# Kernel tuning notes

Measured on AMD Instinct MI355X. Metric: run time of the kernel, lower is better.

## Reference

```python
import jax, jax.numpy as jnp
import numpy as np

NK, NV, DK, DV = 16, 32, 128, 128
R = NV // NK
KCONV, CHUNK = 4, 64
KEY_DIM, VALUE_DIM = NK * DK, NV * DV
CONV_DIM = 2 * KEY_DIM + VALUE_DIM
HIDDEN = 2048
B, S = 1, 4096


def _l2norm(x, eps=1e-6):
    return x * jax.lax.rsqrt(jnp.sum(x * x, -1, keepdims=True) + eps)


def _causal_dwconv(x, w):
    # x: [B, C, S], w: [C, K]; depthwise causal conv (pad K-1 on left),
    # equivalent to torch F.conv1d(groups=C, padding=K-1)[..., :S]
    K = w.shape[-1]
    T = x.shape[-1]
    xp = jnp.pad(x, ((0, 0), (0, 0), (K - 1, 0)))
    out = jnp.zeros_like(x)
    for j in range(K):  # fixed tiny kernel taps
        out = out + w[None, :, j, None] * xp[:, :, j:j + T]
    return out


def _chunk_gated_delta_rule(q, k, v, g, beta):
    # q,k: [B,S,H,DK], v: [B,S,H,DV], g,beta: [B,S,H]; S % CHUNK == 0
    dtype0 = q.dtype
    q = _l2norm(q)
    k = _l2norm(k)
    tr = lambda x: jnp.swapaxes(x, 1, 2).astype(jnp.float32)
    q, k, v = tr(q), tr(k), tr(v)
    g = jnp.swapaxes(g, 1, 2).astype(jnp.float32)
    beta = jnp.swapaxes(beta, 1, 2).astype(jnp.float32)
    Bb, H, T, dk = k.shape
    dv = v.shape[-1]
    N = T // CHUNK
    q = q * dk ** -0.5
    v_beta = v * beta[..., None]
    k_beta = k * beta[..., None]
    resh = lambda x: x.reshape(Bb, H, N, CHUNK, x.shape[-1])
    q, k, v, k_beta, v_beta = map(resh, (q, k, v, k_beta, v_beta))
    g = jnp.cumsum(g.reshape(Bb, H, N, CHUNK), axis=-1)
    lo = jnp.tril(jnp.ones((CHUNK, CHUNK), bool))
    lo_strict = jnp.tril(jnp.ones((CHUNK, CHUNK), bool), -1)
    gdiff = g[..., :, None] - g[..., None, :]
    decay = jnp.where(lo, jnp.exp(jnp.where(lo, gdiff, 0.0)), 0.0)  # [B,H,N,C,C]
    # strictly-lower M = tril_{-1}(k_beta @ k^T * decay); the original in-chunk
    # forward-substitution loop computes exactly (I + M)^{-1}
    M = jnp.where(lo_strict, jnp.einsum('bhnik,bhnjk->bhnij', k_beta, k) * decay, 0.0)
    eye = jnp.eye(CHUNK, dtype=jnp.float32)
    T_inv = jax.scipy.linalg.solve_triangular(
        eye + M, jnp.broadcast_to(eye, M.shape), lower=True, unit_diagonal=True)
    v_c = jnp.einsum('bhnij,bhnjv->bhniv', T_inv, v_beta)
    k_cumdecay = jnp.einsum('bhnij,bhnjk->bhnik', T_inv, k_beta * jnp.exp(g)[..., None])
    attn_local = jnp.where(lo, jnp.einsum('bhnik,bhnjk->bhnij', q, k) * decay, 0.0)
    mv = lambda x: jnp.moveaxis(x, 2, 0)  # chunk axis to front for scan
    xs = (mv(q), mv(k), mv(v_c), mv(g), mv(attn_local), mv(k_cumdecay))
    S0 = jnp.zeros((Bb, H, dk, dv), jnp.float32)

    def step(state, inp):
        q_i, k_i, v_i, g_i, attn_i, kcd_i = inp
        g_last = g_i[..., -1]  # [B,H]
        v_prime = jnp.einsum('bhik,bhkv->bhiv', kcd_i, state)
        v_new = v_i - v_prime
        attn_inter = jnp.einsum('bhik,bhkv->bhiv', q_i * jnp.exp(g_i)[..., None], state)
        out_i = attn_inter + jnp.einsum('bhij,bhjv->bhiv', attn_i, v_new)
        k_dec = k_i * jnp.exp(g_last[..., None] - g_i)[..., None]
        new_state = state * jnp.exp(g_last)[..., None, None] + \
            jnp.einsum('bhik,bhiv->bhkv', k_dec, v_new)
        return new_state, out_i

    _, outs = jax.lax.scan(step, S0, xs)  # [N,B,H,C,DV]
    core = jnp.moveaxis(outs, 0, 2).reshape(Bb, H, T, dv)
    return jnp.swapaxes(core, 1, 2).astype(dtype0)


def _forward(hidden_states, W_qkvz, W_ba, conv_w, dt_bias, A_log, norm_weight, W_out):
    Bx, Sx, _ = hidden_states.shape
    qkvz = (hidden_states @ W_qkvz).reshape(Bx, Sx, NK, 2 * DK + 2 * R * DV)
    ba = (hidden_states @ W_ba).reshape(Bx, Sx, NK, 2 * R)
    q = qkvz[..., :DK]
    k = qkvz[..., DK:2 * DK]
    v = qkvz[..., 2 * DK:2 * DK + R * DV].reshape(Bx, Sx, NV, DV)
    z = qkvz[..., 2 * DK + R * DV:].reshape(Bx, Sx, NV, DV)
    b = ba[..., :R].reshape(Bx, Sx, NV)
    a = ba[..., R:].reshape(Bx, Sx, NV)
    mixed = jnp.concatenate(
        [q.reshape(Bx, Sx, -1), k.reshape(Bx, Sx, -1), v.reshape(Bx, Sx, -1)], axis=-1)
    mixed = jax.nn.silu(_causal_dwconv(jnp.swapaxes(mixed, 1, 2), conv_w))
    mixed = jnp.swapaxes(mixed, 1, 2)
    q = mixed[..., :KEY_DIM].reshape(Bx, Sx, NK, DK)
    k = mixed[..., KEY_DIM:2 * KEY_DIM].reshape(Bx, Sx, NK, DK)
    v = mixed[..., 2 * KEY_DIM:].reshape(Bx, Sx, NV, DV)
    beta = jax.nn.sigmoid(b)
    g = -jnp.exp(A_log.astype(jnp.float32)) * jax.nn.softplus(
        a.astype(jnp.float32) + dt_bias.astype(jnp.float32))
    q = jnp.repeat(q, R, axis=2)  # GQA: expand k-heads to v-heads
    k = jnp.repeat(k, R, axis=2)
    core = _chunk_gated_delta_rule(q, k, v, g, beta)  # [B,S,NV,DV]
    h = core.astype(jnp.float32)
    h = h * jax.lax.rsqrt(jnp.mean(h * h, axis=-1, keepdims=True) + 1e-6)
    h = norm_weight * h
    h = h * jax.nn.silu(z.astype(jnp.float32))
    return h.reshape(Bx, Sx, VALUE_DIM) @ W_out


def setup_inputs() -> dict:
    ks = jax.random.split(jax.random.key(0), 8)
    return {
        'hidden_states': jax.random.normal(ks[0], (B, S, HIDDEN), jnp.float32),
        'W_qkvz': jax.random.normal(ks[1], (HIDDEN, 2 * KEY_DIM + 2 * VALUE_DIM), jnp.float32) * 0.02,
        'W_ba': jax.random.normal(ks[2], (HIDDEN, 2 * NV), jnp.float32) * 0.02,
        'conv_w': jax.random.normal(ks[3], (CONV_DIM, KCONV), jnp.float32) * 0.2,
        'dt_bias': jax.random.normal(ks[4], (NV,), jnp.float32) * 0.1,
        'A_log': jax.random.normal(ks[5], (NV,), jnp.float32) * 0.1,
        'norm_weight': jnp.ones((DV,), jnp.float32),
        'W_out': jax.random.normal(ks[6], (VALUE_DIM, HIDDEN), jnp.float32) * 0.02,
    }


def reference(hidden_states, W_qkvz, W_ba, conv_w, dt_bias, A_log, norm_weight, W_out):
    return _forward(hidden_states, W_qkvz, W_ba, conv_w, dt_bias, A_log, norm_weight, W_out)
```

## Files before the change

### kernel.cpp

```cpp
#include <hip/hip_runtime.h>

typedef unsigned short u16;
typedef __attribute__((ext_vector_type(2))) float f32x2;
typedef __attribute__((ext_vector_type(4))) float f32x4;
typedef __attribute__((ext_vector_type(2))) u16 u16x2;
typedef __attribute__((ext_vector_type(4))) u16 u16x4;
typedef __attribute__((ext_vector_type(8))) u16 u16x8;
typedef __attribute__((ext_vector_type(8))) __bf16 bf16x8;

__device__ __forceinline__ float bf2f(u16 u){ unsigned v = ((unsigned)u) << 16; return __builtin_bit_cast(float, v); }
__device__ __forceinline__ u16 f2bf(float f){
  unsigned u = __builtin_bit_cast(unsigned, f);
  u += 0x7fffu + ((u >> 16) & 1u);
  return (u16)(u >> 16);
}
__device__ __forceinline__ f32x4 b4f(u16x4 u){
  f32x4 r; r[0] = bf2f(u[0]); r[1] = bf2f(u[1]); r[2] = bf2f(u[2]); r[3] = bf2f(u[3]); return r;
}
__device__ __forceinline__ u16x4 p4(f32x4 v){
  u16x4 o; o[0] = f2bf(v[0]); o[1] = f2bf(v[1]); o[2] = f2bf(v[2]); o[3] = f2bf(v[3]); return o;
}
__device__ __forceinline__ void gld16(const void* g, const void* l){
  __builtin_amdgcn_global_load_lds((__attribute__((address_space(1))) void*)(void*)g,
                                   (__attribute__((address_space(3))) void*)(void*)l, 16, 0, 0);
}
__device__ __forceinline__ float sigmoidf(float x){ return 1.f / (1.f + expf(-x)); }
__device__ __forceinline__ float siluf(float x){ return x / (1.f + expf(-x)); }

__global__ __launch_bounds__(256) void k_cast(const float* __restrict__ in, u16* __restrict__ out, int n4){
  int t = blockIdx.x * 256 + threadIdx.x;
  if (t >= n4) return;
  f32x4 v = ((const f32x4*)in)[t];
  u16x4 o;
  o[0] = f2bf(v[0]); o[1] = f2bf(v[1]); o[2] = f2bf(v[2]); o[3] = f2bf(v[3]);
  ((u16x4*)out)[t] = o;
}

template<int PERM>
__global__ __launch_bounds__(256) void k_trans(const float* __restrict__ in, u16* __restrict__ out, int K, int N){
  __shared__ float tile[32][33];
  int tx = threadIdx.x, ty = threadIdx.y;
  int n0 = blockIdx.x * 32, k0 = blockIdx.y * 32;
  #pragma unroll
  for (int j = 0; j < 32; j += 8) tile[ty + j][tx] = in[(size_t)(k0 + ty + j) * N + n0 + tx];
  __syncthreads();
  #pragma unroll
  for (int j = 0; j < 32; j += 8){
    int n = n0 + ty + j;
    int np;
    if (PERM){
      int g = n / 768, r = n - g * 768;
      np = (r < 512) ? (g * 512 + r) : (8192 + g * 256 + (r - 512));
    } else np = n;
    out[(size_t)np * K + k0 + tx] = f2bf(tile[tx][ty + j]);
  }
}

template<int MODE>
__global__ __launch_bounds__(256) void k_gemm(const u16* __restrict__ A, const u16* __restrict__ Bt,
                                              void* __restrict__ C, void* __restrict__ C2, int N, int K){
  __shared__ u16 As[128 * 32];
  __shared__ u16 Bs[128 * 32];
  const int tid = threadIdx.x;
  const int wave = tid >> 6, lane = tid & 63;
  const int gm = blockIdx.y * 128, gn = blockIdx.x * 128;
  const int c0 = wave * 2, c1 = c0 + 1;
  const int r0 = c0 * 16 + (lane >> 2), r1 = r0 + 16;
  const int kp = (lane & 3) * 8;
  const u16* a0 = A + (size_t)(gm + r0) * K + kp;
  const u16* a1 = A + (size_t)(gm + r1) * K + kp;
  const u16* b0 = Bt + (size_t)(gn + r0) * K + kp;
  const u16* b1 = Bt + (size_t)(gn + r1) * K + kp;
  const int wr = (wave >> 1) * 64, wc = (wave & 1) * 64;
  f32x4 acc[4][4];
  #pragma unroll
  for (int m = 0; m < 4; m++)
    #pragma unroll
    for (int n = 0; n < 4; n++) acc[m][n] = 0.f;
  for (int k0 = 0; k0 < K; k0 += 32){
    __syncthreads();
    gld16(a0 + k0, &As[c0 * 512]);
    gld16(a1 + k0, &As[c1 * 512]);
    gld16(b0 + k0, &Bs[c0 * 512]);
    gld16(b1 + k0, &Bs[c1 * 512]);
    __syncthreads();
    bf16x8 af[4], bfv[4];
    #pragma unroll
    for (int m = 0; m < 4; m++)
      af[m] = __builtin_bit_cast(bf16x8, *(const u16x8*)&As[(wr + m * 16 + (lane & 15)) * 32 + (lane >> 4) * 8]);
    #pragma unroll
    for (int n = 0; n < 4; n++)
      bfv[n] = __builtin_bit_cast(bf16x8, *(const u16x8*)&Bs[(wc + n * 16 + (lane & 15)) * 32 + (lane >> 4) * 8]);
    #pragma unroll
    for (int m = 0; m < 4; m++)
      #pragma unroll
      for (int n = 0; n < 4; n++)
        acc[m][n] = __builtin_amdgcn_mfma_f32_16x16x32_bf16(af[m], bfv[n], acc[m][n], 0, 0, 0);
  }
  #pragma unroll
  for (int m = 0; m < 4; m++){
    int row = gm + wr + m * 16 + (lane >> 4) * 4;
    #pragma unroll
    for (int n = 0; n < 4; n++){
      int col = gn + wc + n * 16 + (lane & 15);
      #pragma unroll
      for (int j = 0; j < 4; j++){
        if (MODE == 0){
          ((float*)C)[(size_t)(row + j) * N + col] = acc[m][n][j];
        } else {
          if (col < 8192) ((u16*)C)[(size_t)(row + j) * 8192 + col]         = f2bf(acc[m][n][j]);
          else            ((u16*)C2)[(size_t)(row + j) * 4096 + col - 8192] = f2bf(acc[m][n][j]);
        }
      }
    }
  }
}

__global__ __launch_bounds__(256) void k_ba(const float* __restrict__ hs, const float* __restrict__ Wba,
                                            float* __restrict__ ba){
  int wave = threadIdx.x >> 6, lane = threadIdx.x & 63;
  int s0 = (blockIdx.x * 4 + wave) * 4;
  f32x4 acc = 0.f;
  for (int k = 0; k < 2048; k += 4){
    float w0 = Wba[(size_t)(k + 0) * 64 + lane];
    float w1 = Wba[(size_t)(k + 1) * 64 + lane];
    float w2 = Wba[(size_t)(k + 2) * 64 + lane];
    float w3 = Wba[(size_t)(k + 3) * 64 + lane];
    f32x4 h0 = *(const f32x4*)&hs[(size_t)(s0 + 0) * 2048 + k];
    f32x4 h1 = *(const f32x4*)&hs[(size_t)(s0 + 1) * 2048 + k];
    f32x4 h2 = *(const f32x4*)&hs[(size_t)(s0 + 2) * 2048 + k];
    f32x4 h3 = *(const f32x4*)&hs[(size_t)(s0 + 3) * 2048 + k];
    acc[0] += h0[0]*w0 + h0[1]*w1 + h0[2]*w2 + h0[3]*w3;
    acc[1] += h1[0]*w0 + h1[1]*w1 + h1[2]*w2 + h1[3]*w3;
    acc[2] += h2[0]*w0 + h2[1]*w1 + h2[2]*w2 + h2[3]*w3;
    acc[3] += h3[0]*w0 + h3[1]*w1 + h3[2]*w2 + h3[3]*w3;
  }
  #pragma unroll
  for (int r = 0; r < 4; r++) ba[(size_t)(s0 + r) * 64 + lane] = acc[r];
}

__global__ __launch_bounds__(256) void k_conv(const u16* __restrict__ qkvB, const float* __restrict__ cw,
                                              float* __restrict__ qcF, float* __restrict__ kcF, u16* __restrict__ vcB){
  int idx = blockIdx.x * 256 + threadIdx.x;
  int c8 = idx & 1023, s = idx >> 10;
  int c = c8 * 8;
  int col;
  if (c < 2048)      { int hh = c >> 7, d = c & 127; col = hh * 512 + d; }
  else if (c < 4096) { int cc = c - 2048, hh = cc >> 7, d = cc & 127; col = hh * 512 + 128 + d; }
  else               { int cc = c - 4096, nv = cc >> 7, d = cc & 127; col = (nv >> 1) * 512 + 256 + (nv & 1) * 128 + d; }
  float w[8][4];
  #pragma unroll
  for (int e = 0; e < 8; e++){
    f32x4 wv = *(const f32x4*)&cw[(size_t)(c + e) * 4];
    #pragma unroll
    for (int j = 0; j < 4; j++) w[e][j] = wv[j];
  }
  float acc[8] = {0.f,0.f,0.f,0.f,0.f,0.f,0.f,0.f};
  #pragma unroll
  for (int j = 0; j < 4; j++){
    int sp = s - 3 + j;
    if (sp < 0) continue;
    u16x8 x = *(const u16x8*)&qkvB[(size_t)sp * 8192 + col];
    #pragma unroll
    for (int e = 0; e < 8; e++) acc[e] += w[e][j] * bf2f(x[e]);
  }
  if (c < 4096){
    float* outp = (c < 2048) ? qcF + (size_t)s * 2048 + c : kcF + (size_t)s * 2048 + (c - 2048);
    f32x4 oa, ob;
    #pragma unroll
    for (int e = 0; e < 4; e++) oa[e] = siluf(acc[e]);
    #pragma unroll
    for (int e = 0; e < 4; e++) ob[e] = siluf(acc[e + 4]);
    *(f32x4*)&outp[0] = oa;
    *(f32x4*)&outp[4] = ob;
  } else {
    u16x8 ov;
    #pragma unroll
    for (int e = 0; e < 8; e++) ov[e] = f2bf(siluf(acc[e]));
    *(u16x8*)&vcB[(size_t)s * 4096 + (c - 4096)] = ov;
  }
}

__global__ __launch_bounds__(256) void k_bg(const float* __restrict__ ba, const float* __restrict__ Alog,
                                            const float* __restrict__ dtb, float* __restrict__ betaO,
                                            float* __restrict__ gO){
  int idx = blockIdx.x * 256 + threadIdx.x;
  int s = idx >> 5, nv = idx & 31;
  float b = ba[(size_t)s * 64 + (nv >> 1) * 4 + (nv & 1)];
  float a = ba[(size_t)s * 64 + (nv >> 1) * 4 + 2 + (nv & 1)];
  betaO[idx] = sigmoidf(b);
  float x = a + dtb[nv];
  float sp = (x > 20.f) ? x : log1pf(expf(x));
  gO[idx] = -expf(Alog[nv]) * sp;
}

__global__ __launch_bounds__(256) void k_rownorm(const float* __restrict__ qcF, const float* __restrict__ kcF,
                                                 u16* __restrict__ qcB, u16* __restrict__ kcB){
  int wave = threadIdx.x >> 6, lane = threadIdx.x & 63;
  int row = blockIdx.x * 4 + wave;
  const float* src = (row < 65536) ? qcF + (size_t)row * 128 : kcF + (size_t)(row - 65536) * 128;
  u16* dst = (row < 65536) ? qcB + (size_t)row * 128 : kcB + (size_t)(row - 65536) * 128;
  float sc = (row < 65536) ? 0.08838834764831845f : 1.f;
  f32x2 v = ((const f32x2*)src)[lane];
  float ss = v[0] * v[0] + v[1] * v[1];
  #pragma unroll
  for (int off = 32; off; off >>= 1) ss += __shfl_xor(ss, off);
  float inv = rsqrtf(ss + 1e-6f) * sc;
  u16x2 o; o[0] = f2bf(v[0] * inv); o[1] = f2bf(v[1] * inv);
  ((u16x2*)dst)[lane] = o;
}

__global__ __launch_bounds__(256) void k_pre(const u16* __restrict__ qcB, const u16* __restrict__ kcB,
    const u16* __restrict__ vcB, const float* __restrict__ betaB, const float* __restrict__ gB,
    char* __restrict__ scanA, char* __restrict__ scanBg, u16* __restrict__ vcrG){
  __shared__ float sK[64 * 132];
  __shared__ float sX[64 * 264];
  __shared__ float sM[64 * 68];
  __shared__ float sG[64];
  __shared__ float sEg[64];
  __shared__ float sBeta[64];
  float* sQ = sX;
  const int tid = threadIdx.x;
  const int nv = blockIdx.x & 31, chunk = blockIdx.x >> 5;
  const int h = nv >> 1, s0 = chunk * 64;
  char* gA = scanA + ((size_t)nv * 64 + chunk) * 25600;
  u16* kcdG = (u16*)gA;
  u16* attnG = (u16*)(gA + 16384);
  float* egG = (float*)(gA + 24576);
  char* gB2 = scanBg + ((size_t)h * 64 + chunk) * 32768;
  u16* qG  = (u16*)gB2;
  u16* ktG = (u16*)(gB2 + 16384);
  if (tid < 64){
    float g = gB[(size_t)(s0 + tid) * 32 + nv];
    #pragma unroll
    for (int off = 1; off < 64; off <<= 1){ float nb = __shfl_up(g, off); if (tid >= off) g += nb; }
    sG[tid] = g;
    float g63 = __shfl(g, 63);
    float eg = expf(g);
    sEg[tid] = eg;
    egG[tid] = eg;
    egG[64 + tid] = expf(g63 - g);
  } else if (tid < 128){
    sBeta[tid - 64] = betaB[(size_t)(s0 + tid - 64) * 32 + nv];
  }
  for (int t = tid; t < 2048; t += 256){
    int i = t >> 5, d = (t & 31) * 4;
    *(f32x4*)&sK[i * 132 + d] = b4f(*(const u16x4*)&kcB[(size_t)(s0 + i) * 2048 + h * 128 + d]);
    *(f32x4*)&sQ[i * 132 + d] = b4f(*(const u16x4*)&qcB[(size_t)(s0 + i) * 2048 + h * 128 + d]);
  }
  __syncthreads();
  const int jb = tid & 15, ib = tid >> 4;
  float mA[4][4] = {}, aA[4][4] = {};
  for (int k = 0; k < 128; k += 4){
    f32x4 kA[4], qA[4], kB[4];
    #pragma unroll
    for (int r = 0; r < 4; r++){
      kA[r] = *(const f32x4*)&sK[(ib * 4 + r) * 132 + k];
      qA[r] = *(const f32x4*)&sQ[(ib * 4 + r) * 132 + k];
      kB[r] = *(const f32x4*)&sK[(jb * 4 + r) * 132 + k];
    }
    #pragma unroll
    for (int r = 0; r < 4; r++)
      #pragma unroll
      for (int c2 = 0; c2 < 4; c2++)
        #pragma unroll
        for (int kk = 0; kk < 4; kk++){
          mA[r][c2] += kA[r][kk] * kB[c2][kk];
          aA[r][c2] += qA[r][kk] * kB[c2][kk];
        }
  }
  #pragma unroll
  for (int r = 0; r < 4; r++){
    int i = ib * 4 + r;
    float gi = sG[i], bi = sBeta[i];
    f32x4 mrow;
    u16x4 arow;
    #pragma unroll
    for (int c2 = 0; c2 < 4; c2++){
      int j = jb * 4 + c2;
      float dec = expf(gi - sG[j]);
      mrow[c2] = (i > j)  ? mA[r][c2] * bi * dec : 0.f;
      arow[c2] = f2bf((i >= j) ? aA[r][c2] * dec : 0.f);
    }
    *(f32x4*)&sM[i * 68 + jb * 4] = mrow;
    *(u16x4*)&attnG[i * 64 + ((jb * 4) ^ ((i & 7) << 3))] = arow;
  }
  if (!(nv & 1)){
    for (int t = tid; t < 2048; t += 256){
      int i = t >> 5, d = (t & 31) * 4;
      f32x4 qv = *(const f32x4*)&sQ[i * 132 + d];
      u16x4 o; o[0]=f2bf(qv[0]); o[1]=f2bf(qv[1]); o[2]=f2bf(qv[2]); o[3]=f2bf(qv[3]);
      *(u16x4*)&qG[i * 128 + (d ^ ((i & 7) << 3))] = o;
    }
    for (int t = tid; t < 2048; t += 256){
      int k = t & 127, i0 = (t >> 7) * 4;
      u16x4 o;
      #pragma unroll
      for (int r = 0; r < 4; r++) o[r] = f2bf(sK[(i0 + r) * 132 + k]);
      *(u16x4*)&ktG[k * 64 + (i0 ^ ((k & 7) << 3))] = o;
    }
  }
  __syncthreads();
  for (int t = tid; t < 2048; t += 256){
    int i = t >> 5, d = (t & 31) * 4;
    float bi = sBeta[i];
    f32x4 v = b4f(*(const u16x4*)&vcB[(size_t)(s0 + i) * 4096 + nv * 128 + d]);
    v *= bi;
    *(f32x4*)&sX[i * 264 + d] = v;
    f32x4 kb = *(const f32x4*)&sK[i * 132 + d];
    kb *= bi * sEg[i];
    *(f32x4*)&sX[i * 264 + 128 + d] = kb;
  }
  __syncthreads();
  float x[64];
  #pragma unroll
  for (int i = 0; i < 64; i++) x[i] = sX[i * 264 + tid];
  #pragma unroll
  for (int i = 1; i < 64; i++){
    #pragma unroll
    for (int j = 0; j < i; j++) x[i] -= sM[i * 68 + j] * x[j];
  }
  #pragma unroll
  for (int i = 0; i < 64; i++) sX[i * 264 + tid] = x[i];
  __syncthreads();
  for (int t = tid; t < 2048; t += 256){
    int i = t >> 5, d = (t & 31) * 4;
    u16x4 b; b[0]=f2bf(sX[i*264+128+d]); b[1]=f2bf(sX[i*264+128+d+1]); b[2]=f2bf(sX[i*264+128+d+2]); b[3]=f2bf(sX[i*264+128+d+3]);
    *(u16x4*)&kcdG[i * 128 + (d ^ ((i & 7) << 3))] = b;
  }
  u16* vcrBlk = vcrG + ((size_t)nv * 64 + chunk) * 8192;
  for (int t = tid; t < 2048; t += 256){
    int vcol = t >> 4, m = (t >> 2) & 3, r = t & 3;
    int i0 = m * 16 + r * 4;
    u16x4 a;
    #pragma unroll
    for (int j = 0; j < 4; j++) a[j] = f2bf(sX[(i0 + j) * 264 + vcol]);
    *(u16x4*)&vcrBlk[(((m * 8 + (vcol >> 4)) * 64) + r * 16 + (vcol & 15)) * 4] = a;
  }
}

__device__ __forceinline__ void scan_chunk(
    const char* CURB, char* OTHB, u16x4* VCUR, u16x4* VOTH, int CH,
    const char* scanA, const char* scanBg, const u16* vcrG, u16* coreB,
    u16* sST, u16* sVnT, u16* sVeT, f32x4* S,
    int nv, int h, int vg, int wave, int lane, int vgrp, int myv, int swv){
  const int vl = lane & 15, kg = lane >> 4;
  if (CH + 1 < 64){
    const char* gA = scanA + ((size_t)nv * 64 + CH + 1) * 25600;
    for (int slot = wave; slot < 25; slot += 4)
      gld16(gA + slot * 1024 + lane * 16, OTHB + slot * 1024);
    const char* gB2 = scanBg + ((size_t)h * 64 + CH + 1) * 32768;
    for (int slot = wave; slot < 32; slot += 4)
      gld16(gB2 + slot * 1024 + lane * 16, OTHB + 25600 + slot * 1024);
    const u16* vc = vcrG + ((size_t)nv * 64 + CH + 1) * 8192;
    #pragma unroll
    for (int m = 0; m < 4; m++)
      VOTH[m] = *(const u16x4*)&vc[((m * 8 + vgrp) * 64 + lane) * 4];
  }
  const u16* kcdL  = (const u16*)(CURB);
  const u16* attnL = (const u16*)(CURB + 16384);
  const float* egL = (const float*)(CURB + 24576);
  const u16* qL    = (const u16*)(CURB + 25600);
  const u16* ktL   = (const u16*)(CURB + 25600 + 16384);
  f32x4 vp[4], ai[4];
  #pragma unroll
  for (int m = 0; m < 4; m++){ vp[m] = 0.f; ai[m] = 0.f; }
  #pragma unroll
  for (int kt = 0; kt < 4; kt++){
    int ko = kt * 32 + kg * 8;
    bf16x8 sf = __builtin_bit_cast(bf16x8, *(const u16x8*)&sST[myv * 128 + (ko ^ swv)]);
    #pragma unroll
    for (int m = 0; m < 4; m++){
      int row = m * 16 + vl, rs = (row & 7) << 3;
      bf16x8 kf = __builtin_bit_cast(bf16x8, *(const u16x8*)&kcdL[row * 128 + (ko ^ rs)]);
      vp[m] = __builtin_amdgcn_mfma_f32_16x16x32_bf16(kf, sf, vp[m], 0, 0, 0);
      bf16x8 qf = __builtin_bit_cast(bf16x8, *(const u16x8*)&qL[row * 128 + (ko ^ rs)]);
      ai[m] = __builtin_amdgcn_mfma_f32_16x16x32_bf16(qf, sf, ai[m], 0, 0, 0);
    }
  }
  float eL = egL[63];
  #pragma unroll
  for (int m = 0; m < 4; m++){
    f32x4 vn = b4f(VCUR[m]) - vp[m];
    f32x4 ed4 = *(const f32x4*)&egL[64 + m * 16 + kg * 4];
    f32x4 eg4 = *(const f32x4*)&egL[m * 16 + kg * 4];
    int ja = (m * 16 + kg * 4) ^ swv;
    *(u16x4*)&sVnT[myv * 64 + ja] = p4(vn);
    *(u16x4*)&sVeT[myv * 64 + ja] = p4(vn * ed4);
    ai[m] *= eg4;
  }
  #pragma unroll
  for (int ms = 0; ms < 8; ms++) S[ms] *= eL;
  #pragma unroll
  for (int jt = 0; jt < 2; jt++){
    int jo = jt * 32 + kg * 8;
    bf16x8 vnf = __builtin_bit_cast(bf16x8, *(const u16x8*)&sVnT[myv * 64 + (jo ^ swv)]);
    bf16x8 vef = __builtin_bit_cast(bf16x8, *(const u16x8*)&sVeT[myv * 64 + (jo ^ swv)]);
    #pragma unroll
    for (int m = 0; m < 4; m++){
      int row = m * 16 + vl, rs = (row & 7) << 3;
      bf16x8 af = __builtin_bit_cast(bf16x8, *(const u16x8*)&attnL[row * 64 + (jo ^ rs)]);
      ai[m] = __builtin_amdgcn_mfma_f32_16x16x32_bf16(af, vnf, ai[m], 0, 0, 0);
    }
    #pragma unroll
    for (int ms = 0; ms < 8; ms++){
      int krow = ms * 16 + vl, rs = (krow & 7) << 3;
      bf16x8 kf = __builtin_bit_cast(bf16x8, *(const u16x8*)&ktL[krow * 64 + (jo ^ rs)]);
      S[ms] = __builtin_amdgcn_mfma_f32_16x16x32_bf16(kf, vef, S[ms], 0, 0, 0);
    }
  }
  #pragma unroll
  for (int m = 0; m < 4; m++){
    size_t ig = (size_t)CH * 64 + m * 16 + kg * 4;
    size_t base = (ig * 32 + nv) * 128 + vg * 64 + wave * 16 + vl;
    #pragma unroll
    for (int j = 0; j < 4; j++) coreB[base + (size_t)j * 4096] = f2bf(ai[m][j]);
  }
  #pragma unroll
  for (int ms = 0; ms < 8; ms++){
    int k0 = ms * 16 + kg * 4;
    *(u16x4*)&sST[myv * 128 + (k0 ^ swv)] = p4(S[ms]);
  }
  __syncthreads();
}

__global__ __launch_bounds__(256) void k_scan(const char* __restrict__ scanA, const char* __restrict__ scanBg,
    const u16* __restrict__ vcrG, u16* __restrict__ coreB){
  __shared__ alignas(16) char sbuf[2 * 58368];
  __shared__ alignas(16) u16 sST[64 * 128];
  __shared__ alignas(16) u16 sVnT[64 * 64];
  __shared__ alignas(16) u16 sVeT[64 * 64];
  const int tid = threadIdx.x;
  const int wave = tid >> 6, lane = tid & 63;
  const int nv = blockIdx.x & 31, vg = blockIdx.x >> 5;
  const int h = nv >> 1;
  const int vgrp = vg * 4 + wave;
  const int myv = wave * 16 + (lane & 15);
  const int swv = (myv & 7) << 3;
  for (int t = tid; t < 8192; t += 256) sST[t] = 0;
  f32x4 S[8];
  #pragma unroll
  for (int ms = 0; ms < 8; ms++) S[ms] = 0.f;
  u16x4 vA[4], vB[4];
  {
    const char* gA = scanA + (size_t)(nv * 64) * 25600;
    for (int slot = wave; slot < 25; slot += 4)
      gld16(gA + slot * 1024 + lane * 16, sbuf + slot * 1024);
    const char* gB2 = scanBg + (size_t)(h * 64) * 32768;
    for (int slot = wave; slot < 32; slot += 4)
      gld16(gB2 + slot * 1024 + lane * 16, sbuf + 25600 + slot * 1024);
    const u16* vc = vcrG + (size_t)(nv * 64) * 8192;
    #pragma unroll
    for (int m = 0; m < 4; m++)
      vA[m] = *(const u16x4*)&vc[((m * 8 + vgrp) * 64 + lane) * 4];
  }
  __syncthreads();
  for (int c = 0; c < 64; c += 2){
    scan_chunk(sbuf,         sbuf + 58368, vA, vB, c,
               scanA, scanBg, vcrG, coreB, sST, sVnT, sVeT, S,
               nv, h, vg, wave, lane, vgrp, myv, swv);
    scan_chunk(sbuf + 58368, sbuf,         vB, vA, c + 1,
               scanA, scanBg, vcrG, coreB, sST, sVnT, sVeT, S,
               nv, h, vg, wave, lane, vgrp, myv, swv);
  }
}

__global__ __launch_bounds__(256) void k_gate(const u16* __restrict__ coreB, const u16* __restrict__ zB,
                                              const float* __restrict__ nw, u16* __restrict__ hb){
  int wave = threadIdx.x >> 6, lane = threadIdx.x & 63;
  int row = blockIdx.x * 4 + wave;
  int s = row >> 5, nv = row & 31;
  u16x2 cu = *(const u16x2*)&coreB[(size_t)row * 128 + lane * 2];
  float c0 = bf2f(cu[0]), c1 = bf2f(cu[1]);
  float ss = c0 * c0 + c1 * c1;
  #pragma unroll
  for (int off = 32; off; off >>= 1) ss += __shfl_xor(ss, off);
  float rms = rsqrtf(ss * (1.f / 128.f) + 1e-6f);
  int zcol = (nv >> 1) * 256 + (nv & 1) * 128 + lane * 2;
  u16x2 zu = *(const u16x2*)&zB[(size_t)s * 4096 + zcol];
  float z0 = siluf(bf2f(zu[0])), z1 = siluf(bf2f(zu[1]));
  u16x2 ho;
  ho[0] = f2bf(c0 * rms * nw[lane * 2]     * z0);
  ho[1] = f2bf(c1 * rms * nw[lane * 2 + 1] * z1);
  *(u16x2*)&hb[(size_t)row * 128 + lane * 2] = ho;
}

extern "C" void kernel_launch(void* const* d_in, const int* in_sizes, int n_in,
                              void* d_out, int out_size, void* d_ws, size_t ws_size,
                              hipStream_t stream){
  (void)in_sizes; (void)n_in; (void)out_size; (void)ws_size;
  const float* hs    = (const float*)d_in[0];
  const float* Wqkvz = (const float*)d_in[1];
  const float* Wba   = (const float*)d_in[2];
  const float* cw    = (const float*)d_in[3];
  const float* dtb   = (const float*)d_in[4];
  const float* Alog  = (const float*)d_in[5];
  const float* nw    = (const float*)d_in[6];
  const float* Wout  = (const float*)d_in[7];
  char* ws = (char*)d_ws;
  const size_t MB = 1ull << 20;
  u16*   hsb   = (u16*)  (ws + 0);
  u16*   wqT   = (u16*)  (ws + 16 * MB);
  float* qcF   = (float*)(ws + 0);
  u16*   vcrG  = (u16*)  (ws + 0);
  u16*   hb    = (u16*)  (ws + 0);
  u16*   vcB   = (u16*)  (ws + 32 * MB);
  u16*   qkvB  = (u16*)  (ws + 64 * MB);
  char*  scanA =         (ws + 64 * MB);
  float* ba    = (float*)(ws + 114 * MB);
  float* betaB = (float*)(ws + 115 * MB);
  float* gB    = (float*)(ws + 115 * MB + 512 * 1024);
  u16*   zB    = (u16*)  (ws + 128 * MB);
  u16*   qcB   = (u16*)  (ws + 160 * MB);
  u16*   kcB   = (u16*)  (ws + 176 * MB);
  u16*   coreB = (u16*)  (ws + 160 * MB);
  float* kcF   = (float*)(ws + 192 * MB);
  char*  scanBg=         (ws + 192 * MB);
  u16*   woT   = (u16*)  (ws + 192 * MB);
  float* out   = (float*)d_out;

  k_cast<<<8192, 256, 0, stream>>>(hs, hsb, 2097152);
  k_trans<1><<<dim3(384, 64), dim3(32, 8), 0, stream>>>(Wqkvz, wqT, 2048, 12288);
  k_gemm<2><<<dim3(96, 32), 256, 0, stream>>>(hsb, wqT, qkvB, zB, 12288, 2048);
  k_conv<<<16384, 256, 0, stream>>>(qkvB, cw, qcF, kcF, vcB);
  k_ba<<<256, 256, 0, stream>>>(hs, Wba, ba);
  k_bg<<<512, 256, 0, stream>>>(ba, Alog, dtb, betaB, gB);
  k_rownorm<<<32768, 256, 0, stream>>>(qcF, kcF, qcB, kcB);
  k_pre<<<2048, 256, 0, stream>>>(qcB, kcB, vcB, betaB, gB, scanA, scanBg, vcrG);
  k_scan<<<64, 256, 0, stream>>>(scanA, scanBg, vcrG, coreB);
  k_gate<<<32768, 256, 0, stream>>>(coreB, zB, nw, hb);
  k_trans<0><<<dim3(64, 128), dim3(32, 8), 0, stream>>>(Wout, woT, 4096, 2048);
  k_gemm<0><<<dim3(16, 32), 256, 0, stream>>>(hb, woT, out, nullptr, 2048, 4096);
}
```

Baseline: 1.369 ms.

## Replace QKVZ projection GEMM with 256x256 tiled, double-buffered, swizzled MFMA kernel

```diff
diff --git a/kernel.cpp b/kernel.cpp
--- a/kernel.cpp
+++ b/kernel.cpp
@@ -26,6 +26,8 @@
 }
 __device__ __forceinline__ float sigmoidf(float x){ return 1.f / (1.f + expf(-x)); }
 __device__ __forceinline__ float siluf(float x){ return x / (1.f + expf(-x)); }
+
+#define GBAR() do { asm volatile("" ::: "memory"); __builtin_amdgcn_s_barrier(); asm volatile("" ::: "memory"); } while(0)
 
 __global__ __launch_bounds__(256) void k_cast(const float* __restrict__ in, u16* __restrict__ out, int n4){
   int t = blockIdx.x * 256 + threadIdx.x;
@@ -57,13 +59,134 @@
 }
 
 template<int MODE>
+__global__ __launch_bounds__(512) void k_gemm256(const u16* __restrict__ A, const u16* __restrict__ Bt,
+                                                 void* __restrict__ C, void* __restrict__ C2, int N, int K){
+  __shared__ alignas(16) char lds[131072];
+  const int tid = threadIdx.x;
+  const int wid = tid >> 6, lane = tid & 63;
+  const int vl = lane & 15, kg = lane >> 4;
+  const int wm = wid >> 2, wn = wid & 3;
+  const int nwg = (int)gridDim.x;
+  const int swzb = ((int)blockIdx.x & 7) * (nwg >> 3) + ((int)blockIdx.x >> 3);
+  const int nbx = N >> 8;
+  const int bx = swzb % nbx, by = swzb / nbx;
+  const int gm = by << 8, gn = bx << 8;
+  const int nt = K >> 6;
+
+  auto stageA = [&](int t, int h){
+    if (t >= nt) return;
+    const int k0 = t << 6;
+    char* slot = lds + ((t & 1) * 2 + h) * 16384;
+    #pragma unroll
+    for (int p = 0; p < 2; p++){
+      int o = p * 8192 + wid * 1024 + lane * 16;
+      int sr = o >> 7, cs = (o >> 4) & 7;
+      int gr = gm + ((sr >> 6) << 7) + h * 64 + (sr & 63);
+      int gc = k0 + ((cs ^ (sr & 7)) << 3);
+      gld16(A + (size_t)gr * K + gc, slot + p * 8192 + wid * 1024);
+    }
+  };
+  auto stageB = [&](int t, int h){
+    if (t >= nt) return;
+    const int k0 = t << 6;
+    char* slot = lds + 65536 + ((t & 1) * 2 + h) * 16384;
+    #pragma unroll
+    for (int p = 0; p < 2; p++){
+      int o = p * 8192 + wid * 1024 + lane * 16;
+      int sr = o >> 7, cs = (o >> 4) & 7;
+      int gr = gn + ((sr >> 5) << 6) + h * 32 + (sr & 31);
+      int gc = k0 + ((cs ^ (sr & 7)) << 3);
+      gld16(Bt + (size_t)gr * K + gc, slot + p * 8192 + wid * 1024);
+    }
+  };
+
+  f32x4 acc[8][4];
+  #pragma unroll
+  for (int a = 0; a < 8; a++)
+    #pragma unroll
+    for (int b = 0; b < 4; b++) acc[a][b] = 0.f;
+
+  stageA(0, 0); stageB(0, 0); stageA(0, 1); stageB(0, 1); stageA(1, 0); stageB(1, 0);
+  asm volatile("s_waitcnt vmcnt(8)" ::: "memory");
+  GBAR();
+
+#define PHASE(MH, NH, STAGECALL, VMSEL) do { \
+    const char* Asl_ = lds + ((cur * 2 + (MH)) * 16384); \
+    const char* Bsl_ = lds + 65536 + ((cur * 2 + (NH)) * 16384); \
+    bf16x8 af_[4][2], bf_[2][2]; \
+    _Pragma("unroll") \
+    for (int mi = 0; mi < 4; mi++){ \
+      int sr = wm * 64 + mi * 16 + vl; \
+      _Pragma("unroll") \
+      for (int ks = 0; ks < 2; ks++) \
+        af_[mi][ks] = __builtin_bit_cast(bf16x8, *(const u16x8*)(Asl_ + sr * 128 + (((ks * 4 + kg) ^ (vl & 7)) << 4))); \
+    } \
+    _Pragma("unroll") \
+    for (int ni = 0; ni < 2; ni++){ \
+      int br = wn * 32 + ni * 16 + vl; \
+      _Pragma("unroll") \
+      for (int ks = 0; ks < 2; ks++) \
+        bf_[ni][ks] = __builtin_bit_cast(bf16x8, *(const u16x8*)(Bsl_ + br * 128 + (((ks * 4 + kg) ^ (vl & 7)) << 4))); \
+    } \
+    STAGECALL; \
+    __builtin_amdgcn_s_setprio(1); \
+    _Pragma("unroll") \
+    for (int mi = 0; mi < 4; mi++) \
+      _Pragma("unroll") \
+      for (int ni = 0; ni < 2; ni++) \
+        _Pragma("unroll") \
+        for (int ks = 0; ks < 2; ks++) \
+          acc[(MH) * 4 + mi][(NH) * 2 + ni] = __builtin_amdgcn_mfma_f32_16x16x32_bf16(af_[mi][ks], bf_[ni][ks], acc[(MH) * 4 + mi][(NH) * 2 + ni], 0, 0, 0); \
+    __builtin_amdgcn_s_setprio(0); \
+    VMSEL; \
+    GBAR(); \
+  } while (0)
+
+  for (int t = 0; t < nt; t++){
+    const int cur = t & 1;
+    const bool tail = (t >= nt - 3);
+    PHASE(0, 0, stageA(t + 1, 1),
+          { if (!tail) asm volatile("s_waitcnt vmcnt(6)" ::: "memory");
+            else       asm volatile("s_waitcnt vmcnt(0)" ::: "memory"); });
+    PHASE(0, 1, stageB(t + 1, 1), {});
+    PHASE(1, 0, stageA(t + 2, 0), {});
+    PHASE(1, 1, stageB(t + 2, 0),
+          { if (!tail) asm volatile("s_waitcnt vmcnt(8)" ::: "memory");
+            else       asm volatile("s_waitcnt vmcnt(0)" ::: "memory"); });
+  }
+#undef PHASE
+
+  #pragma unroll
+  for (int a = 0; a < 8; a++){
+    int row = gm + wm * 128 + (a >> 2) * 64 + (a & 3) * 16 + (lane >> 4) * 4;
+    #pragma unroll
+    for (int b = 0; b < 4; b++){
+      int col = gn + wn * 64 + (b >> 1) * 32 + (b & 1) * 16 + vl;
+      #pragma unroll
+      for (int j = 0; j < 4; j++){
+        if (MODE == 0){
+          ((float*)C)[(size_t)(row + j) * N + col] = acc[a][b][j];
+        } else {
+          if (col < 8192) ((u16*)C)[(size_t)(row + j) * 8192 + col]         = f2bf(acc[a][b][j]);
+          else            ((u16*)C2)[(size_t)(row + j) * 4096 + col - 8192] = f2bf(acc[a][b][j]);
+        }
+      }
+    }
+  }
+}
+
+template<int MODE>
 __global__ __launch_bounds__(256) void k_gemm(const u16* __restrict__ A, const u16* __restrict__ Bt,
                                               void* __restrict__ C, void* __restrict__ C2, int N, int K){
   __shared__ u16 As[128 * 32];
   __shared__ u16 Bs[128 * 32];
   const int tid = threadIdx.x;
   const int wave = tid >> 6, lane = tid & 63;
-  const int gm = blockIdx.y * 128, gn = blockIdx.x * 128;
+  const int nbx = (int)gridDim.x;
+  const int nwg = nbx * (int)gridDim.y;
+  const int linear = (int)blockIdx.y * nbx + (int)blockIdx.x;
+  const int swz = (linear & 7) * (nwg >> 3) + (linear >> 3);
+  const int gm = (swz / nbx) * 128, gn = (swz % nbx) * 128;
   const int c0 = wave * 2, c1 = c0 + 1;
   const int r0 = c0 * 16 + (lane >> 2), r1 = r0 + 16;
   const int kp = (lane & 3) * 8;
@@ -521,7 +644,7 @@
 
   k_cast<<<8192, 256, 0, stream>>>(hs, hsb, 2097152);
   k_trans<1><<<dim3(384, 64), dim3(32, 8), 0, stream>>>(Wqkvz, wqT, 2048, 12288);
-  k_gemm<2><<<dim3(96, 32), 256, 0, stream>>>(hsb, wqT, qkvB, zB, 12288, 2048);
+  k_gemm256<2><<<768, 512, 0, stream>>>(hsb, wqT, qkvB, zB, 12288, 2048);
   k_conv<<<16384, 256, 0, stream>>>(qkvB, cw, qcF, kcF, vcB);
   k_ba<<<256, 256, 0, stream>>>(hs, Wba, ba);
   k_bg<<<512, 256, 0, stream>>>(ba, Alog, dtb, betaB, gB);
```

After: 1.295 ms. 5.4% less time.
